# Kernel optimization log

Measured on AMD Instinct MI355X. Metric: run time of the kernel, lower is better.

The kernel has to match this reference:

```python
import jax, jax.numpy as jnp
import numpy as np

NUM_HEADS = 16
ROPE_BASE = 10000.0
NEG_INF = float('-inf')


def _rotate_half_interleaved(x):
    # x: [..., d]; interleaved rotation: (-x2, x1) pairs
    x1 = x[..., ::2]
    x2 = x[..., 1::2]
    return jnp.stack((-x2, x1), axis=-1).reshape(x.shape)


def _rope_tables(seq_len, head_dim, dtype):
    inv_freq = 1.0 / (ROPE_BASE ** (jnp.arange(0, head_dim, 2, dtype=jnp.float32) / head_dim))
    pos = jnp.arange(seq_len, dtype=jnp.float32)
    freqs = pos[:, None] * inv_freq[None, :]          # [S, d/2]
    emb = jnp.concatenate((freqs, freqs), axis=-1)    # [S, d]  (HF-style concat, as in source)
    return jnp.cos(emb).astype(dtype), jnp.sin(emb).astype(dtype)


def setup_inputs() -> dict:
    key = jax.random.key(0)
    ks = jax.random.split(key, 4)
    B, S, H = 2, 2048, 2048
    scale = 0.02
    x = jax.random.normal(ks[0], (B, S, H), dtype=jnp.float32)
    qkv_w = jax.random.normal(ks[1], (3 * H, H), dtype=jnp.float32) * scale
    qkv_b = jnp.zeros((3 * H,), dtype=jnp.float32)
    out_w = jax.random.normal(ks[2], (H, H), dtype=jnp.float32) * scale
    out_b = jnp.zeros((H,), dtype=jnp.float32)
    attention_mask = jnp.ones((B, S), dtype=jnp.int32)
    return {"x": x, "attention_mask": attention_mask, "qkv_w": qkv_w,
            "qkv_b": qkv_b, "out_w": out_w, "out_b": out_b}


def reference(x, attention_mask, qkv_w, qkv_b, out_w, out_b):
    B, S, H = x.shape
    nh = NUM_HEADS
    hd = H // nh
    scale = hd ** -0.5

    qkv = x @ qkv_w.T + qkv_b                            # [B,S,3H]
    qkv = qkv.reshape(B, S, 3, nh, hd).transpose(2, 0, 3, 1, 4)  # [3,B,nh,S,hd]
    q, k, v = qkv[0], qkv[1], qkv[2]

    cos, sin = _rope_tables(S, hd, x.dtype)              # [S,hd]
    cos = cos[None, None, :, :]
    sin = sin[None, None, :, :]
    q = q * cos + _rotate_half_interleaved(q) * sin
    k = k * cos + _rotate_half_interleaved(k) * sin

    scores = jnp.einsum('bhqd,bhkd->bhqk', q, k) * scale  # [B,nh,S,S]
    causal = jnp.triu(jnp.ones((S, S), dtype=bool), k=1)
    scores = jnp.where(causal[None, None], NEG_INF, scores)
    key_mask = (attention_mask == 0)[:, None, None, :]    # [B,1,1,S]
    scores = jnp.where(key_mask, NEG_INF, scores)

    weights = jax.nn.softmax(scores, axis=-1)
    attn = jnp.einsum('bhqk,bhkd->bhqd', weights, v)       # [B,nh,S,hd]
    attn = attn.transpose(0, 2, 1, 3).reshape(B, S, H)
    return attn @ out_w.T + out_b
```

## Files before the change

kernel.cpp:

```cpp
#include <hip/hip_runtime.h>

typedef __bf16 bf16;
typedef __bf16 bf16x4 __attribute__((ext_vector_type(4)));
typedef __bf16 bf16x8 __attribute__((ext_vector_type(8)));
typedef float f32x4 __attribute__((ext_vector_type(4)));
typedef float f32x16 __attribute__((ext_vector_type(16)));

#define MFMA_BF16(a, b, c) __builtin_amdgcn_mfma_f32_16x16x32_bf16(a, b, c, 0, 0, 0)
#define MFMA32(a, b, c)    __builtin_amdgcn_mfma_f32_32x32x16_bf16(a, b, c, 0, 0, 0)

__device__ __forceinline__ void async16(const void* g, void* l) {
    __builtin_amdgcn_global_load_lds(
        (const __attribute__((address_space(1))) void*)g,
        (__attribute__((address_space(3))) void*)l,
        16, 0, 0);
}

__global__ void cvt8(const float* __restrict__ in, bf16* __restrict__ out, int n) {
    int i = (blockIdx.x * 256 + threadIdx.x) * 8;
    if (i >= n) return;
    float4 a = *(const float4*)(in + i);
    float4 b = *(const float4*)(in + i + 4);
    bf16x8 o;
    o[0] = (bf16)a.x; o[1] = (bf16)a.y; o[2] = (bf16)a.z; o[3] = (bf16)a.w;
    o[4] = (bf16)b.x; o[5] = (bf16)b.y; o[6] = (bf16)b.z; o[7] = (bf16)b.w;
    *(bf16x8*)(out + i) = o;
}

__global__ void tables_k(const int* __restrict__ am, float* __restrict__ cosT,
                         float* __restrict__ sinT, float* __restrict__ mbias) {
    int i = blockIdx.x * 256 + threadIdx.x;
    int s = i >> 7, d = i & 127, fi = d & 63;
    float inv = exp2f(-(float)fi * (13.287712379549449f / 64.0f));
    float ang = (float)s * inv;
    cosT[i] = cosf(ang);
    sinT[i] = sinf(ang);
    if (i < 2 * 2048) mbias[i] = (am[i] == 0) ? -1e30f : 0.0f;
}

template <int EPI>
__global__ void __launch_bounds__(256, 2)
gemm_bt(const bf16* __restrict__ A, const bf16* __restrict__ Bt,
        const float* __restrict__ bias, float* __restrict__ Cf,
        bf16* __restrict__ qb, bf16* __restrict__ kb, bf16* __restrict__ vtb,
        const float* __restrict__ cosT, const float* __restrict__ sinT,
        int M, int N, int K, int bn0) {
    __shared__ __align__(16) bf16 sA[128 * 64];
    __shared__ __align__(16) bf16 sB[128 * 64];
    const int tid  = threadIdx.x;
    const int lane = tid & 63;
    const int quad = lane >> 4, l15 = lane & 15;
    const int wid = tid >> 6, wm = wid >> 1, wn = wid & 1;
    const int bm = blockIdx.x, bn = blockIdx.y + bn0;

    f32x4 acc[4][4];
#pragma unroll
    for (int i = 0; i < 4; i++)
#pragma unroll
        for (int j = 0; j < 4; j++)
#pragma unroll
            for (int c = 0; c < 4; c++) acc[i][j][c] = 0.0f;

    const int r0 = tid >> 3, x0 = tid & 7;
    const int g0 = x0 ^ (r0 & 7);
    const bf16* pa = A  + (size_t)(bm * 128 + r0) * K + g0 * 8;
    const bf16* pb = Bt + (size_t)(bn * 128 + r0) * K + g0 * 8;
    bf16* la = sA + tid * 8;
    bf16* lb = sB + tid * 8;
    const size_t gstep = (size_t)32 * K;

    for (int k0 = 0; k0 < K; k0 += 64) {
#pragma unroll
        for (int i = 0; i < 4; i++) {
            async16(pa + i * gstep, la + i * 2048);
            async16(pb + i * gstep, lb + i * 2048);
        }
        pa += 64; pb += 64;
        __syncthreads();
#pragma unroll
        for (int ks = 0; ks < 2; ks++) {
            bf16x8 af[4], bfr[4];
#pragma unroll
            for (int i = 0; i < 4; i++) {
                int r = wm * 64 + i * 16 + l15;
                int x = (ks * 4 + quad) ^ (r & 7);
                af[i] = *(const bf16x8*)(sA + r * 64 + x * 8);
            }
#pragma unroll
            for (int i = 0; i < 4; i++) {
                int r = wn * 64 + i * 16 + l15;
                int x = (ks * 4 + quad) ^ (r & 7);
                bfr[i] = *(const bf16x8*)(sB + r * 64 + x * 8);
            }
#pragma unroll
            for (int mi = 0; mi < 4; mi++)
#pragma unroll
                for (int ni = 0; ni < 4; ni++)
                    acc[mi][ni] = MFMA_BF16(af[mi], bfr[ni], acc[mi][ni]);
        }
        __syncthreads();
    }

    if (EPI == 0) {
#pragma unroll
        for (int mi = 0; mi < 4; mi++)
#pragma unroll
            for (int ni = 0; ni < 4; ni++) {
                int row0 = bm * 128 + wm * 64 + mi * 16 + quad * 4;
                int col  = bn * 128 + wn * 64 + ni * 16 + l15;
                float bv = bias[col];
#pragma unroll
                for (int r = 0; r < 4; r++)
                    Cf[(size_t)(row0 + r) * N + col] = acc[mi][ni][r] + bv;
            }
    } else {
#pragma unroll
        for (int mi = 0; mi < 4; mi++)
#pragma unroll
            for (int ni = 0; ni < 4; ni++) {
                int col   = bn * 128 + wn * 64 + ni * 16 + l15;
                int which = col >> 11;
                int hcol  = col & 2047;
                int h = hcol >> 7, d = hcol & 127;
                float bv = bias[col];
#pragma unroll
                for (int r = 0; r < 4; r++) {
                    int row = bm * 128 + wm * 64 + mi * 16 + quad * 4 + r;
                    int b = row >> 11, s = row & 2047;
                    float v  = acc[mi][ni][r] + bv;
                    float vp = __shfl_xor(v, 1, 64);
                    float ov = v;
                    if (which < 2) {
                        float c  = cosT[(s << 7) + d];
                        float sn = sinT[(s << 7) + d];
                        ov = v * c + ((d & 1) ? vp : -vp) * sn;
                    }
                    if (which == 0) ov *= 0.08838834764831845f;
                    size_t bh = (size_t)(b * 16 + h);
                    if (which == 0)      qb[(bh * 2048 + s) * 128 + d] = (bf16)ov;
                    else if (which == 1) kb[(bh * 2048 + s) * 128 + d] = (bf16)ov;
                    else                 vtb[(bh * 128 + d) * 2048 + s] = (bf16)ov;
                }
            }
    }
}

__global__ void __launch_bounds__(256, 2)
fattn(const bf16* __restrict__ Q, const bf16* __restrict__ Kg,
      const bf16* __restrict__ Vt, const float* __restrict__ mbias,
      bf16* __restrict__ O) {
    __shared__ __align__(16) bf16 sK[2][64 * 128];
    __shared__ __align__(16) bf16 sV[2][128 * 64];
    __shared__ __align__(16) bf16 sP[4 * 32 * 64];
    const int tid = threadIdx.x, lane = tid & 63, w = tid >> 6;
    const int l31 = lane & 31, half = lane >> 5;
    const int bx = (int)blockIdx.x;
    const int qt = (bx & 1) ? 15 - (bx >> 1) : (bx >> 1);
    const int bh = blockIdx.y, b = bh >> 4, hh = bh & 15;
    const int myq = qt * 128 + w * 32 + l31;

    const bf16* Qb  = Q  + (size_t)bh * 2048 * 128;
    const bf16* Kbh = Kg + (size_t)bh * 2048 * 128;
    const bf16* Vbh = Vt + (size_t)bh * 128 * 2048;
    const float* mbb = mbias + b * 2048;
    bf16* sPw = sP + w * 2048;

    bf16x8 qf[8];
#pragma unroll
    for (int kq = 0; kq < 8; kq++)
        qf[kq] = *(const bf16x8*)(Qb + (size_t)myq * 128 + kq * 16 + half * 8);

    f32x16 oacc[4];
#pragma unroll
    for (int dt = 0; dt < 4; dt++)
#pragma unroll
        for (int c = 0; c < 16; c++) oacc[dt][c] = 0.0f;
    float m_s = -3e38f, l_s = 0.0f;

    const int rk = tid >> 4, xk = tid & 15, gk = xk ^ (rk & 15);
    const int rv = tid >> 3, xv = tid & 7,  gv = xv ^ (rv & 7);
    const int nkt = 2 * qt + 2;

#pragma unroll
    for (int i = 0; i < 4; i++) {
        async16(Kbh + (size_t)(rk + i * 16) * 128 + gk * 8, &sK[0][(i * 256 + tid) * 8]);
        async16(Vbh + (size_t)(rv + i * 32) * 2048 + gv * 8, &sV[0][(i * 256 + tid) * 8]);
    }
    __syncthreads();

    for (int kt = 0; kt < nkt; kt++) {
        const int kb0 = kt * 64;
        const int buf = kt & 1;
        if (kt + 1 < nkt) {
            const int nb0 = kb0 + 64;
#pragma unroll
            for (int i = 0; i < 4; i++) {
                async16(Kbh + (size_t)(nb0 + rk + i * 16) * 128 + gk * 8,
                        &sK[buf ^ 1][(i * 256 + tid) * 8]);
                async16(Vbh + (size_t)(rv + i * 32) * 2048 + nb0 + gv * 8,
                        &sV[buf ^ 1][(i * 256 + tid) * 8]);
            }
        }
        const bf16* sKb = sK[buf];
        const bf16* sVb = sV[buf];

        f32x16 sacc[2];
#pragma unroll
        for (int t = 0; t < 2; t++)
#pragma unroll
            for (int c = 0; c < 16; c++) sacc[t][c] = 0.0f;
#pragma unroll
        for (int kq = 0; kq < 8; kq++) {
#pragma unroll
            for (int t = 0; t < 2; t++) {
                int row = t * 32 + l31;
                int x = (kq * 2 + half) ^ (row & 15);
                bf16x8 kf = *(const bf16x8*)(sKb + row * 128 + x * 8);
                sacc[t] = MFMA32(kf, qf[kq], sacc[t]);
            }
        }

        float ps[2][16];
        float mx = -3e38f;
#pragma unroll
        for (int t = 0; t < 2; t++)
#pragma unroll
            for (int g = 0; g < 4; g++) {
                float4 mb4 = *(const float4*)(mbb + kb0 + t * 32 + 8 * g + 4 * half);
#pragma unroll
                for (int r2 = 0; r2 < 4; r2++) {
                    int sk = kb0 + t * 32 + 8 * g + 4 * half + r2;
                    float v = sacc[t][g * 4 + r2] + ((const float*)&mb4)[r2];
                    v = (sk > myq) ? -1e30f : v;
                    ps[t][g * 4 + r2] = v;
                    mx = fmaxf(mx, v);
                }
            }

        mx = fmaxf(mx, __shfl_xor(mx, 32, 64));
        float mnew  = fmaxf(m_s, mx);
        float alpha = __expf(m_s - mnew);
        float rs = 0.0f;
#pragma unroll
        for (int t = 0; t < 2; t++)
#pragma unroll
            for (int c = 0; c < 16; c++) {
                float p = __expf(ps[t][c] - mnew);
                ps[t][c] = p;
                rs += p;
            }
        l_s = l_s * alpha + rs;
        m_s = mnew;
#pragma unroll
        for (int dt = 0; dt < 4; dt++) oacc[dt] *= alpha;

#pragma unroll
        for (int t = 0; t < 2; t++)
#pragma unroll
            for (int g = 0; g < 4; g++) {
                int c = t * 4 + g;
                int x = c ^ (l31 & 7);
                bf16x4 p4;
#pragma unroll
                for (int r2 = 0; r2 < 4; r2++) p4[r2] = (bf16)ps[t][g * 4 + r2];
                *(bf16x4*)(sPw + l31 * 64 + x * 8 + half * 4) = p4;
            }

#pragma unroll
        for (int kq2 = 0; kq2 < 4; kq2++) {
            int cp = kq2 * 2 + half;
            int xp = cp ^ (l31 & 7);
            bf16x8 pf = *(const bf16x8*)(sPw + l31 * 64 + xp * 8);
#pragma unroll
            for (int dt = 0; dt < 4; dt++) {
                int row = dt * 32 + l31;
                int xv2 = cp ^ (row & 7);
                bf16x8 vf = *(const bf16x8*)(sVb + row * 64 + xv2 * 8);
                oacc[dt] = MFMA32(vf, pf, oacc[dt]);
            }
        }
        __syncthreads();
    }

    l_s += __shfl_xor(l_s, 32, 64);
    float inv = 1.0f / l_s;
    size_t base = ((size_t)(b * 2048 + myq)) * 2048 + hh * 128;
#pragma unroll
    for (int dt = 0; dt < 4; dt++)
#pragma unroll
        for (int g = 0; g < 4; g++) {
            bf16x4 o4;
#pragma unroll
            for (int r2 = 0; r2 < 4; r2++) o4[r2] = (bf16)(oacc[dt][g * 4 + r2] * inv);
            *(bf16x4*)(O + base + dt * 32 + 8 * g + 4 * half) = o4;
        }
}

extern "C" void kernel_launch(void* const* d_in, const int* in_sizes, int n_in,
                              void* d_out, int out_size, void* d_ws, size_t ws_size,
                              hipStream_t stream) {
    const float* x     = (const float*)d_in[0];
    const int*   am    = (const int*)d_in[1];
    const float* qkvw  = (const float*)d_in[2];
    const float* qkvb  = (const float*)d_in[3];
    const float* outw  = (const float*)d_in[4];
    const float* outb  = (const float*)d_in[5];
    float* out = (float*)d_out;

    char* ws = (char*)d_ws;
    bf16*  xb    = (bf16*)(ws);
    bf16*  wqkv  = (bf16*)(ws + (16ull << 20));
    bf16*  wout  = (bf16*)(ws + (40ull << 20));
    bf16*  qb    = (bf16*)(ws + (48ull << 20));
    bf16*  kb    = (bf16*)(ws + (64ull << 20));
    bf16*  vtb   = (bf16*)(ws + (80ull << 20));
    bf16*  attn  = (bf16*)(ws + (96ull << 20));
    float* cosT  = (float*)(ws + (112ull << 20));
    float* sinT  = (float*)(ws + (113ull << 20));
    float* mbias = (float*)(ws + (114ull << 20));

    cvt8<<<4096, 256, 0, stream>>>(x, xb, 4096 * 2048);
    cvt8<<<6144, 256, 0, stream>>>(qkvw, wqkv, 6144 * 2048);
    cvt8<<<2048, 256, 0, stream>>>(outw, wout, 2048 * 2048);
    tables_k<<<1024, 256, 0, stream>>>(am, cosT, sinT, mbias);

    gemm_bt<1><<<dim3(32, 24), 256, 0, stream>>>(
        xb, wqkv, qkvb, nullptr, qb, kb, vtb, cosT, sinT, 4096, 6144, 2048, 0);
    gemm_bt<1><<<dim3(32, 24), 256, 0, stream>>>(
        xb, wqkv, qkvb, nullptr, qb, kb, vtb, cosT, sinT, 4096, 6144, 2048, 24);

    fattn<<<dim3(16, 32), 256, 0, stream>>>(qb, kb, vtb, mbias, attn);

    gemm_bt<0><<<dim3(32, 16), 256, 0, stream>>>(
        attn, wout, outb, out, nullptr, nullptr, nullptr, nullptr, nullptr,
        4096, 2048, 2048, 0);
}
```

Before: 409.0 us.

## Keep attention probabilities in registers, use exp2 softmax, reorder causal tile schedule

The flash-attention kernel no longer round-trips the P tile through shared memory. It packs probabilities to bf16 pairs and exchanges halves with cross-lane shuffles to form the MFMA B operand directly. The softmax scale now folds log2(e) into the Q scaling so exp2f replaces __expf. Fully unmasked tiles skip the causal compare, and the LDS swizzles for K and V are changed to reduce bank conflicts. The grid becomes 1D, scheduling heavy query tiles first then light ones, which relies on the register-shuffle layout matching the MFMA operand layout.

```diff
diff --git a/kernel.cpp b/kernel.cpp
--- a/kernel.cpp
+++ b/kernel.cpp
@@ -1,6 +1,7 @@
 #include <hip/hip_runtime.h>
 
 typedef __bf16 bf16;
+typedef __bf16 bf16x2 __attribute__((ext_vector_type(2)));
 typedef __bf16 bf16x4 __attribute__((ext_vector_type(4)));
 typedef __bf16 bf16x8 __attribute__((ext_vector_type(8)));
 typedef float f32x4 __attribute__((ext_vector_type(4)));
@@ -14,6 +15,11 @@
         (const __attribute__((address_space(1))) void*)g,
         (__attribute__((address_space(3))) void*)l,
         16, 0, 0);
+}
+
+__device__ __forceinline__ unsigned pack2(float a, float b) {
+    bf16x2 t; t[0] = (bf16)a; t[1] = (bf16)b;
+    return __builtin_bit_cast(unsigned, t);
 }
 
 __global__ void cvt8(const float* __restrict__ in, bf16* __restrict__ out, int n) {
@@ -35,7 +41,7 @@
     float ang = (float)s * inv;
     cosT[i] = cosf(ang);
     sinT[i] = sinf(ang);
-    if (i < 2 * 2048) mbias[i] = (am[i] == 0) ? -1e30f : 0.0f;
+    if (i < 2 * 2048) mbias[i] = (am[i] == 0) ? -1.4427e30f : 0.0f;
 }
 
 template <int EPI>
@@ -135,7 +141,7 @@
                         float sn = sinT[(s << 7) + d];
                         ov = v * c + ((d & 1) ? vp : -vp) * sn;
                     }
-                    if (which == 0) ov *= 0.08838834764831845f;
+                    if (which == 0) ov *= 0.12751743f;
                     size_t bh = (size_t)(b * 16 + h);
                     if (which == 0)      qb[(bh * 2048 + s) * 128 + d] = (bf16)ov;
                     else if (which == 1) kb[(bh * 2048 + s) * 128 + d] = (bf16)ov;
@@ -151,19 +157,23 @@
       bf16* __restrict__ O) {
     __shared__ __align__(16) bf16 sK[2][64 * 128];
     __shared__ __align__(16) bf16 sV[2][128 * 64];
-    __shared__ __align__(16) bf16 sP[4 * 32 * 64];
     const int tid = threadIdx.x, lane = tid & 63, w = tid >> 6;
     const int l31 = lane & 31, half = lane >> 5;
-    const int bx = (int)blockIdx.x;
-    const int qt = (bx & 1) ? 15 - (bx >> 1) : (bx >> 1);
-    const int bh = blockIdx.y, b = bh >> 4, hh = bh & 15;
+    const int id = (int)blockIdx.x;
+    const int round = id >> 8, u = id & 255;
+    const int bh = u & 31, j8 = u >> 5;
+    const int qt = round ? j8 : 15 - j8;
+    const int b = bh >> 4, hh = bh & 15;
     const int myq = qt * 128 + w * 32 + l31;
+    const int qmin = qt * 128 + w * 32;
 
     const bf16* Qb  = Q  + (size_t)bh * 2048 * 128;
     const bf16* Kbh = Kg + (size_t)bh * 2048 * 128;
     const bf16* Vbh = Vt + (size_t)bh * 128 * 2048;
     const float* mbb = mbias + b * 2048;
-    bf16* sPw = sP + w * 2048;
+
+    const int swk = (l31 & 15) ^ (l31 >> 4);
+    const int swv = (l31 & 7) ^ ((l31 >> 3) & 3);
 
     bf16x8 qf[8];
 #pragma unroll
@@ -177,14 +187,17 @@
         for (int c = 0; c < 16; c++) oacc[dt][c] = 0.0f;
     float m_s = -3e38f, l_s = 0.0f;
 
-    const int rk = tid >> 4, xk = tid & 15, gk = xk ^ (rk & 15);
-    const int rv = tid >> 3, xv = tid & 7,  gv = xv ^ (rv & 7);
+    const int rk = tid >> 4, xk = tid & 15, gkb = xk ^ rk;
+    const int rv = tid >> 3, xv = tid & 7;
+    const int gv = xv ^ (rv & 7) ^ ((rv >> 3) & 3);
     const int nkt = 2 * qt + 2;
 
 #pragma unroll
     for (int i = 0; i < 4; i++) {
-        async16(Kbh + (size_t)(rk + i * 16) * 128 + gk * 8, &sK[0][(i * 256 + tid) * 8]);
-        async16(Vbh + (size_t)(rv + i * 32) * 2048 + gv * 8, &sV[0][(i * 256 + tid) * 8]);
+        async16(Kbh + (size_t)(rk + i * 16) * 128 + (gkb ^ (i & 1)) * 8,
+                &sK[0][(i * 256 + tid) * 8]);
+        async16(Vbh + (size_t)(rv + i * 32) * 2048 + gv * 8,
+                &sV[0][(i * 256 + tid) * 8]);
     }
     __syncthreads();
 
@@ -195,7 +208,7 @@
             const int nb0 = kb0 + 64;
 #pragma unroll
             for (int i = 0; i < 4; i++) {
-                async16(Kbh + (size_t)(nb0 + rk + i * 16) * 128 + gk * 8,
+                async16(Kbh + (size_t)(nb0 + rk + i * 16) * 128 + (gkb ^ (i & 1)) * 8,
                         &sK[buf ^ 1][(i * 256 + tid) * 8]);
                 async16(Vbh + (size_t)(rv + i * 32) * 2048 + nb0 + gv * 8,
                         &sV[buf ^ 1][(i * 256 + tid) * 8]);
@@ -214,39 +227,53 @@
 #pragma unroll
             for (int t = 0; t < 2; t++) {
                 int row = t * 32 + l31;
-                int x = (kq * 2 + half) ^ (row & 15);
+                int x = (kq * 2 + half) ^ swk;
                 bf16x8 kf = *(const bf16x8*)(sKb + row * 128 + x * 8);
                 sacc[t] = MFMA32(kf, qf[kq], sacc[t]);
             }
         }
 
-        float ps[2][16];
         float mx = -3e38f;
-#pragma unroll
-        for (int t = 0; t < 2; t++)
-#pragma unroll
-            for (int g = 0; g < 4; g++) {
-                float4 mb4 = *(const float4*)(mbb + kb0 + t * 32 + 8 * g + 4 * half);
-#pragma unroll
-                for (int r2 = 0; r2 < 4; r2++) {
-                    int sk = kb0 + t * 32 + 8 * g + 4 * half + r2;
-                    float v = sacc[t][g * 4 + r2] + ((const float*)&mb4)[r2];
-                    v = (sk > myq) ? -1e30f : v;
-                    ps[t][g * 4 + r2] = v;
-                    mx = fmaxf(mx, v);
+        if (kb0 + 63 < qmin) {
+#pragma unroll
+            for (int t = 0; t < 2; t++)
+#pragma unroll
+                for (int g = 0; g < 4; g++) {
+                    float4 mb4 = *(const float4*)(mbb + kb0 + t * 32 + 8 * g + 4 * half);
+#pragma unroll
+                    for (int r2 = 0; r2 < 4; r2++) {
+                        float v = sacc[t][g * 4 + r2] + ((const float*)&mb4)[r2];
+                        sacc[t][g * 4 + r2] = v;
+                        mx = fmaxf(mx, v);
+                    }
                 }
-            }
+        } else {
+#pragma unroll
+            for (int t = 0; t < 2; t++)
+#pragma unroll
+                for (int g = 0; g < 4; g++) {
+                    float4 mb4 = *(const float4*)(mbb + kb0 + t * 32 + 8 * g + 4 * half);
+#pragma unroll
+                    for (int r2 = 0; r2 < 4; r2++) {
+                        int sk = kb0 + t * 32 + 8 * g + 4 * half + r2;
+                        float v = sacc[t][g * 4 + r2] + ((const float*)&mb4)[r2];
+                        v = (sk > myq) ? -1e30f : v;
+                        sacc[t][g * 4 + r2] = v;
+                        mx = fmaxf(mx, v);
+                    }
+                }
+        }
 
         mx = fmaxf(mx, __shfl_xor(mx, 32, 64));
         float mnew  = fmaxf(m_s, mx);
-        float alpha = __expf(m_s - mnew);
+        float alpha = exp2f(m_s - mnew);
         float rs = 0.0f;
 #pragma unroll
         for (int t = 0; t < 2; t++)
 #pragma unroll
             for (int c = 0; c < 16; c++) {
-                float p = __expf(ps[t][c] - mnew);
-                ps[t][c] = p;
+                float p = exp2f(sacc[t][c] - mnew);
+                sacc[t][c] = p;
                 rs += p;
             }
         l_s = l_s * alpha + rs;
@@ -255,28 +282,32 @@
         for (int dt = 0; dt < 4; dt++) oacc[dt] *= alpha;
 
 #pragma unroll
-        for (int t = 0; t < 2; t++)
-#pragma unroll
-            for (int g = 0; g < 4; g++) {
-                int c = t * 4 + g;
-                int x = c ^ (l31 & 7);
-                bf16x4 p4;
-#pragma unroll
-                for (int r2 = 0; r2 < 4; r2++) p4[r2] = (bf16)ps[t][g * 4 + r2];
-                *(bf16x4*)(sPw + l31 * 64 + x * 8 + half * 4) = p4;
-            }
-
-#pragma unroll
-        for (int kq2 = 0; kq2 < 4; kq2++) {
-            int cp = kq2 * 2 + half;
-            int xp = cp ^ (l31 & 7);
-            bf16x8 pf = *(const bf16x8*)(sPw + l31 * 64 + xp * 8);
-#pragma unroll
-            for (int dt = 0; dt < 4; dt++) {
-                int row = dt * 32 + l31;
-                int xv2 = cp ^ (row & 7);
-                bf16x8 vf = *(const bf16x8*)(sVb + row * 64 + xv2 * 8);
-                oacc[dt] = MFMA32(vf, pf, oacc[dt]);
+        for (int t = 0; t < 2; t++) {
+            unsigned w8[8];
+#pragma unroll
+            for (int i = 0; i < 8; i++)
+                w8[i] = pack2(sacc[t][2 * i], sacc[t][2 * i + 1]);
+#pragma unroll
+            for (int s2 = 0; s2 < 2; s2++) {
+                const int bse = 4 * s2;
+                unsigned a0 = half ? w8[bse]     : w8[bse + 2];
+                unsigned a1 = half ? w8[bse + 1] : w8[bse + 3];
+                unsigned z0 = (unsigned)__shfl_xor((int)a0, 32, 64);
+                unsigned z1 = (unsigned)__shfl_xor((int)a1, 32, 64);
+                union { unsigned u[4]; bf16x8 v; } pu;
+                pu.u[0] = half ? z0 : w8[bse];
+                pu.u[1] = half ? z1 : w8[bse + 1];
+                pu.u[2] = half ? w8[bse + 2] : z0;
+                pu.u[3] = half ? w8[bse + 3] : z1;
+                bf16x8 pf = pu.v;
+                const int c = (t * 2 + s2) * 2 + half;
+#pragma unroll
+                for (int dt = 0; dt < 4; dt++) {
+                    int row = dt * 32 + l31;
+                    int x = c ^ swv;
+                    bf16x8 vf = *(const bf16x8*)(sVb + row * 64 + x * 8);
+                    oacc[dt] = MFMA32(vf, pf, oacc[dt]);
+                }
             }
         }
         __syncthreads();
@@ -329,7 +360,7 @@
     gemm_bt<1><<<dim3(32, 24), 256, 0, stream>>>(
         xb, wqkv, qkvb, nullptr, qb, kb, vtb, cosT, sinT, 4096, 6144, 2048, 24);
 
-    fattn<<<dim3(16, 32), 256, 0, stream>>>(qb, kb, vtb, mbias, attn);
+    fattn<<<dim3(512), 256, 0, stream>>>(qb, kb, vtb, mbias, attn);
 
     gemm_bt<0><<<dim3(32, 16), 256, 0, stream>>>(
         attn, wout, outb, out, nullptr, nullptr, nullptr, nullptr, nullptr,
```

After: 409.9 us. No clear change (+0.2%).
